# Performance work log

Hardware: AMD Instinct MI355X
Metric: run time of the kernel (lower is better)

The kernel has to match this reference:

```python
import jax, jax.numpy as jnp
import numpy as np

N_NODES = 50000
N_EDGES = 800000
F_IN = 128
F_OUT = 128
DROP_RATE = 0.6  # torch F.dropout(p=0.6, training=True default)


def setup_inputs() -> dict:
    key = jax.random.key(0)
    k1, k2, k3, k4, k5, k6 = jax.random.split(key, 6)
    x = jax.random.normal(k1, (N_NODES, F_IN), dtype=jnp.float32)
    # edge list: src = center node (sorted, mimics per-node neighbor-list grouping), dst = neighbor
    src = jnp.sort(jax.random.randint(k2, (N_EDGES,), 0, N_NODES, dtype=jnp.int64))
    dst = jax.random.randint(k3, (N_EDGES,), 0, N_NODES, dtype=jnp.int64)
    adj_vals = jax.random.uniform(k4, (N_EDGES,), dtype=jnp.float32)  # normalized adj weights
    stdv = 1.0 / np.sqrt(F_OUT)
    w_mask = jax.random.normal(k5, (2 * F_IN, F_IN), dtype=jnp.float32) * stdv
    w0 = jax.random.uniform(k6, (F_IN, F_OUT), minval=-stdv, maxval=stdv, dtype=jnp.float32)
    return {"x": x, "src": src, "dst": dst, "adj_vals": adj_vals, "w_mask": w_mask, "w0": w0}


def reference(x, src, dst, adj_vals, w_mask, w0):
    # Edge-wise gather of center and neighbor features: [E, F] each
    cen = x[src]
    nei = x[dst]
    # Per-edge mask: sigmoid(concat(center, neighbor) @ W_mask)  -> [E, F]
    m = jax.nn.sigmoid(jnp.concatenate([cen, nei], axis=1) @ w_mask)
    # Dropout p=0.6 (deterministic key for reproducibility), torch-style inverted scaling
    keep = jax.random.bernoulli(jax.random.key(42), 1.0 - DROP_RATE, m.shape)
    m = jnp.where(keep, m / (1.0 - DROP_RATE), jnp.zeros_like(m))
    # Masked weighted neighbor sum per center node, plus the center feature itself
    agg = jax.ops.segment_sum(m * nei, src, num_segments=N_NODES)
    x_new = x + agg
    # Dense projection, then spmm(adj, support) over the same edge structure
    support = x_new @ w0
    out = jax.ops.segment_sum(adj_vals[:, None] * support[dst], src, num_segments=N_NODES)
    return out
```

## Files before the change

kernel.cpp:

```cpp
#include <hip/hip_runtime.h>
#include <stdint.h>


#define NNODES 50000
#define FDIM 128

__device__ __forceinline__ uint32_t rotl32(uint32_t x, int r) {
  return (x << r) | (x >> (32 - r));
}

__device__ __forceinline__ void threefry2x32(uint32_t k0, uint32_t k1,
                                             uint32_t x0, uint32_t x1,
                                             uint32_t& o0, uint32_t& o1) {
  uint32_t k2 = k0 ^ k1 ^ 0x1BD11BDAu;
  x0 += k0; x1 += k1;
  x0 += x1; x1 = rotl32(x1, 13); x1 ^= x0;
  x0 += x1; x1 = rotl32(x1, 15); x1 ^= x0;
  x0 += x1; x1 = rotl32(x1, 26); x1 ^= x0;
  x0 += x1; x1 = rotl32(x1,  6); x1 ^= x0;
  x0 += k1; x1 += k2 + 1u;
  x0 += x1; x1 = rotl32(x1, 17); x1 ^= x0;
  x0 += x1; x1 = rotl32(x1, 29); x1 ^= x0;
  x0 += x1; x1 = rotl32(x1, 16); x1 ^= x0;
  x0 += x1; x1 = rotl32(x1, 24); x1 ^= x0;
  x0 += k2; x1 += k0 + 2u;
  x0 += x1; x1 = rotl32(x1, 13); x1 ^= x0;
  x0 += x1; x1 = rotl32(x1, 15); x1 ^= x0;
  x0 += x1; x1 = rotl32(x1, 26); x1 ^= x0;
  x0 += x1; x1 = rotl32(x1,  6); x1 ^= x0;
  x0 += k0; x1 += k1 + 3u;
  x0 += x1; x1 = rotl32(x1, 17); x1 ^= x0;
  x0 += x1; x1 = rotl32(x1, 29); x1 ^= x0;
  x0 += x1; x1 = rotl32(x1, 16); x1 ^= x0;
  x0 += x1; x1 = rotl32(x1, 24); x1 ^= x0;
  x0 += k1; x1 += k2 + 4u;
  x0 += x1; x1 = rotl32(x1, 13); x1 ^= x0;
  x0 += x1; x1 = rotl32(x1, 15); x1 ^= x0;
  x0 += x1; x1 = rotl32(x1, 26); x1 ^= x0;
  x0 += x1; x1 = rotl32(x1,  6); x1 ^= x0;
  x0 += k2; x1 += k0 + 5u;
  o0 = x0; o1 = x1;
}

__device__ __forceinline__ bool keep_drop(uint32_t idx) {
  uint32_t o0, o1;
  threefry2x32(0u, 42u, 0u, idx, o0, o1);
  return (o0 ^ o1) < 1717987328u;
}

__device__ __forceinline__ float sigmoid_f(float z) {
  float e = __builtin_amdgcn_exp2f(z * -1.44269504088896340736f);
  return __builtin_amdgcn_rcpf(1.0f + e);
}

__device__ __forceinline__ bool detect_i64(const int* p, int n) {
  int i = (n / 2) | 1;
  return p[i] == 0 && p[i + 2] == 0 && p[i + 4] == 0;
}

__device__ __forceinline__ int idx_at(const void* p, int i, bool is64) {
  return is64 ? (int)((const long long*)p)[i] : ((const int*)p)[i];
}

__device__ __forceinline__ int lower_bound_idx(const void* a, int n, bool is64, int v) {
  int lo = 0, hi = n;
  while (lo < hi) {
    int mid = (lo + hi) >> 1;
    if (idx_at(a, mid, is64) < v) lo = mid + 1; else hi = mid;
  }
  return lo;
}

__global__ __launch_bounds__(256) void rowptr_kernel(const void* __restrict__ src, int nE,
                                                     int* __restrict__ rowptr) {
  bool is64 = detect_i64((const int*)src, nE);
  int n = blockIdx.x * blockDim.x + threadIdx.x;
  if (n <= NNODES) rowptr[n] = lower_bound_idx(src, nE, is64, n);
}

__global__ __launch_bounds__(256) void cvt_dst(const void* __restrict__ dst, int nE,
                                               int* __restrict__ dst32) {
  bool is64 = detect_i64((const int*)dst, nE);
  int i = blockIdx.x * blockDim.x + threadIdx.x;
  if (i < nE) {
    int d = idx_at(dst, i, is64);
    dst32[i] = min(max(d, 0), NNODES - 1);
  }
}

#define MMR 16
__global__ __launch_bounds__(128) void matmulAB(const float* __restrict__ in,
                                                const float* __restrict__ W,
                                                float* __restrict__ A,
                                                float* __restrict__ B, int nrows) {
  __shared__ float xs[MMR][FDIM];
  int r0 = blockIdx.x * MMR;
  int t = threadIdx.x;
  #pragma unroll
  for (int r = 0; r < MMR; ++r) {
    int row = r0 + r;
    xs[r][t] = (row < nrows) ? in[row * FDIM + t] : 0.0f;
  }
  __syncthreads();
  float accA[MMR] = {}, accB[MMR] = {};
  for (int k = 0; k < FDIM; k += 4) {
    float wa0 = W[(k + 0) * FDIM + t], wa1 = W[(k + 1) * FDIM + t];
    float wa2 = W[(k + 2) * FDIM + t], wa3 = W[(k + 3) * FDIM + t];
    float wb0 = W[(FDIM + k + 0) * FDIM + t], wb1 = W[(FDIM + k + 1) * FDIM + t];
    float wb2 = W[(FDIM + k + 2) * FDIM + t], wb3 = W[(FDIM + k + 3) * FDIM + t];
    #pragma unroll
    for (int r = 0; r < MMR; ++r) {
      float4 xv = *(const float4*)&xs[r][k];
      accA[r] += xv.x * wa0; accA[r] += xv.y * wa1;
      accA[r] += xv.z * wa2; accA[r] += xv.w * wa3;
      accB[r] += xv.x * wb0; accB[r] += xv.y * wb1;
      accB[r] += xv.z * wb2; accB[r] += xv.w * wb3;
    }
  }
  #pragma unroll
  for (int r = 0; r < MMR; ++r) {
    int row = r0 + r;
    if (row < nrows) { A[row * FDIM + t] = accA[r]; B[row * FDIM + t] = accB[r]; }
  }
}

__global__ __launch_bounds__(128) void matmul16(const float* __restrict__ in,
                                                const float* __restrict__ W,
                                                float* __restrict__ out, int nrows) {
  __shared__ float xs[MMR][FDIM];
  int r0 = blockIdx.x * MMR;
  int t = threadIdx.x;
  #pragma unroll
  for (int r = 0; r < MMR; ++r) {
    int row = r0 + r;
    xs[r][t] = (row < nrows) ? in[row * FDIM + t] : 0.0f;
  }
  __syncthreads();
  float acc[MMR] = {};
  for (int k = 0; k < FDIM; k += 4) {
    float w0 = W[(k + 0) * FDIM + t], w1 = W[(k + 1) * FDIM + t];
    float w2 = W[(k + 2) * FDIM + t], w3 = W[(k + 3) * FDIM + t];
    #pragma unroll
    for (int r = 0; r < MMR; ++r) {
      float4 xv = *(const float4*)&xs[r][k];
      acc[r] += xv.x * w0; acc[r] += xv.y * w1;
      acc[r] += xv.z * w2; acc[r] += xv.w * w3;
    }
  }
  #pragma unroll
  for (int r = 0; r < MMR; ++r) {
    int row = r0 + r;
    if (row < nrows) out[row * FDIM + t] = acc[r];
  }
}

__global__ __launch_bounds__(128) void edge_agg(const float* __restrict__ x,
                                                const int* __restrict__ dst32,
                                                const int* __restrict__ rowptr,
                                                const float* __restrict__ A,
                                                const float* __restrict__ B,
                                                float* __restrict__ x_new) {
  int n = blockIdx.x;
  int f = threadIdx.x;
  int lo = rowptr[n], hi = rowptr[n + 1];
  const float* Bf = B + f;
  const float* xf = x + f;
  float a = A[(n << 7) + f];
  float acc0 = 0.f, acc1 = 0.f, acc2 = 0.f, acc3 = 0.f;
  uint32_t idx = ((uint32_t)lo << 7) + (uint32_t)f;
  int e = lo;
  for (; e + 4 <= hi; e += 4, idx += 512u) {
    int d0 = dst32[e + 0], d1 = dst32[e + 1], d2 = dst32[e + 2], d3 = dst32[e + 3];
    float b0 = Bf[d0 << 7], xv0 = xf[d0 << 7];
    float b1 = Bf[d1 << 7], xv1 = xf[d1 << 7];
    float b2 = Bf[d2 << 7], xv2 = xf[d2 << 7];
    float b3 = Bf[d3 << 7], xv3 = xf[d3 << 7];
    bool k0 = keep_drop(idx);
    bool k1 = keep_drop(idx + 128u);
    bool k2 = keep_drop(idx + 256u);
    bool k3 = keep_drop(idx + 384u);
    float m0 = sigmoid_f(a + b0), m1 = sigmoid_f(a + b1);
    float m2 = sigmoid_f(a + b2), m3 = sigmoid_f(a + b3);
    acc0 += k0 ? (m0 * 2.5f) * xv0 : 0.0f;
    acc1 += k1 ? (m1 * 2.5f) * xv1 : 0.0f;
    acc2 += k2 ? (m2 * 2.5f) * xv2 : 0.0f;
    acc3 += k3 ? (m3 * 2.5f) * xv3 : 0.0f;
  }
  for (; e < hi; ++e, idx += 128u) {
    int d = dst32[e];
    float m = sigmoid_f(a + Bf[d << 7]);
    if (keep_drop(idx)) acc0 += (m * 2.5f) * xf[d << 7];
  }
  float acc = (acc0 + acc1) + (acc2 + acc3);
  x_new[(n << 7) + f] = x[(n << 7) + f] + acc;
}

__global__ __launch_bounds__(128) void edge_out(const float* __restrict__ support,
                                                const int* __restrict__ dst32,
                                                const int* __restrict__ rowptr,
                                                const float* __restrict__ adj,
                                                float* __restrict__ out) {
  int n = blockIdx.x;
  int f = threadIdx.x;
  int lo = rowptr[n], hi = rowptr[n + 1];
  const float* Sf = support + f;
  float a0 = 0.f, a1 = 0.f, a2 = 0.f, a3 = 0.f;
  int e = lo;
  for (; e + 4 <= hi; e += 4) {
    int d0 = dst32[e + 0], d1 = dst32[e + 1], d2 = dst32[e + 2], d3 = dst32[e + 3];
    float w0 = adj[e + 0], w1 = adj[e + 1], w2 = adj[e + 2], w3 = adj[e + 3];
    a0 += w0 * Sf[d0 << 7];
    a1 += w1 * Sf[d1 << 7];
    a2 += w2 * Sf[d2 << 7];
    a3 += w3 * Sf[d3 << 7];
  }
  for (; e < hi; ++e) a0 += adj[e] * Sf[dst32[e] << 7];
  out[(n << 7) + f] = (a0 + a1) + (a2 + a3);
}

extern "C" void kernel_launch(void* const* d_in, const int* in_sizes, int n_in,
                              void* d_out, int out_size, void* d_ws, size_t ws_size,
                              hipStream_t stream) {
  const float* x      = (const float*)d_in[0];
  const void*  src    = d_in[1];
  const void*  dst    = d_in[2];
  const float* adj    = (const float*)d_in[3];
  const float* w_mask = (const float*)d_in[4];
  const float* w0     = (const float*)d_in[5];
  float* out = (float*)d_out;

  int nE = in_sizes[1];
  const size_t NF = (size_t)NNODES * FDIM;

  float* A       = (float*)d_ws;
  float* B       = A + NF;
  float* x_new   = B + NF;
  int*   rowptr  = (int*)(x_new + NF);
  int*   dst32   = rowptr + (NNODES + 1);
  float* support = A;

  rowptr_kernel<<<(NNODES + 256) / 256, 256, 0, stream>>>(src, nE, rowptr);
  cvt_dst<<<(nE + 255) / 256, 256, 0, stream>>>(dst, nE, dst32);
  matmulAB<<<(NNODES + MMR - 1) / MMR, 128, 0, stream>>>(x, w_mask, A, B, NNODES);
  edge_agg<<<NNODES, 128, 0, stream>>>(x, dst32, rowptr, A, B, x_new);
  matmul16<<<(NNODES + MMR - 1) / MMR, 128, 0, stream>>>(x_new, w0, support, NNODES);
  edge_out<<<NNODES, 128, 0, stream>>>(support, dst32, rowptr, adj, out);
}
```

Before: 505.0 us.

## Interleave mask logits with features and software-pipeline edge gathers

The mask matmul now writes B and x interleaved as float2, so the edge aggregation fetches both neighbor values with one 8-byte load instead of two scattered 4-byte loads. Both edge kernels use readfirstlane to keep row bounds and neighbor indices scalar, and prefetch the next batch of gathers (4 edges in aggregation, 8 in output) before computing the current one. Launch bounds now request higher occupancy. This needs extra workspace, with a fallback path when the workspace is too small, and the prefetch registers may limit occupancy.

```diff
diff --git a/kernel.cpp b/kernel.cpp
--- a/kernel.cpp
+++ b/kernel.cpp
@@ -53,6 +53,8 @@
   return __builtin_amdgcn_rcpf(1.0f + e);
 }
 
+__device__ __forceinline__ int rfl(int v) { return __builtin_amdgcn_readfirstlane(v); }
+
 __device__ __forceinline__ bool detect_i64(const int* p, int n) {
   int i = (n / 2) | 1;
   return p[i] == 0 && p[i + 2] == 0 && p[i + 4] == 0;
@@ -89,10 +91,11 @@
 }
 
 #define MMR 16
-__global__ __launch_bounds__(128) void matmulAB(const float* __restrict__ in,
-                                                const float* __restrict__ W,
-                                                float* __restrict__ A,
-                                                float* __restrict__ B, int nrows) {
+template <bool USE_BX>
+__global__ __launch_bounds__(128) void matmulAB_k(const float* __restrict__ in,
+                                                  const float* __restrict__ W,
+                                                  float* __restrict__ A,
+                                                  float* __restrict__ Bout, int nrows) {
   __shared__ float xs[MMR][FDIM];
   int r0 = blockIdx.x * MMR;
   int t = threadIdx.x;
@@ -120,7 +123,11 @@
   #pragma unroll
   for (int r = 0; r < MMR; ++r) {
     int row = r0 + r;
-    if (row < nrows) { A[row * FDIM + t] = accA[r]; B[row * FDIM + t] = accB[r]; }
+    if (row < nrows) {
+      A[row * FDIM + t] = accA[r];
+      if (USE_BX) ((float2*)Bout)[(row << 7) + t] = make_float2(accB[r], xs[r][t]);
+      else        Bout[row * FDIM + t] = accB[r];
+    }
   }
 }
 
@@ -154,67 +161,121 @@
   }
 }
 
-__global__ __launch_bounds__(128) void edge_agg(const float* __restrict__ x,
-                                                const int* __restrict__ dst32,
-                                                const int* __restrict__ rowptr,
-                                                const float* __restrict__ A,
-                                                const float* __restrict__ B,
-                                                float* __restrict__ x_new) {
+template <bool USE_BX>
+__global__ __launch_bounds__(128, 4) void edge_agg_k(const float* __restrict__ x,
+                                                     const float* __restrict__ BorBX,
+                                                     const int* __restrict__ dst32,
+                                                     const int* __restrict__ rowptr,
+                                                     const float* __restrict__ A,
+                                                     float* __restrict__ x_new) {
   int n = blockIdx.x;
   int f = threadIdx.x;
-  int lo = rowptr[n], hi = rowptr[n + 1];
-  const float* Bf = B + f;
-  const float* xf = x + f;
+  int lo = rfl(rowptr[n]);
+  int hi = rfl(rowptr[n + 1]);
+  const float2* BX2 = (const float2*)BorBX;
+  const float*  Bf  = BorBX + f;
+  const float*  xf  = x + f;
   float a = A[(n << 7) + f];
   float acc0 = 0.f, acc1 = 0.f, acc2 = 0.f, acc3 = 0.f;
-  uint32_t idx = ((uint32_t)lo << 7) + (uint32_t)f;
   int e = lo;
-  for (; e + 4 <= hi; e += 4, idx += 512u) {
-    int d0 = dst32[e + 0], d1 = dst32[e + 1], d2 = dst32[e + 2], d3 = dst32[e + 3];
-    float b0 = Bf[d0 << 7], xv0 = xf[d0 << 7];
-    float b1 = Bf[d1 << 7], xv1 = xf[d1 << 7];
-    float b2 = Bf[d2 << 7], xv2 = xf[d2 << 7];
-    float b3 = Bf[d3 << 7], xv3 = xf[d3 << 7];
-    bool k0 = keep_drop(idx);
-    bool k1 = keep_drop(idx + 128u);
-    bool k2 = keep_drop(idx + 256u);
-    bool k3 = keep_drop(idx + 384u);
-    float m0 = sigmoid_f(a + b0), m1 = sigmoid_f(a + b1);
-    float m2 = sigmoid_f(a + b2), m3 = sigmoid_f(a + b3);
-    acc0 += k0 ? (m0 * 2.5f) * xv0 : 0.0f;
-    acc1 += k1 ? (m1 * 2.5f) * xv1 : 0.0f;
-    acc2 += k2 ? (m2 * 2.5f) * xv2 : 0.0f;
-    acc3 += k3 ? (m3 * 2.5f) * xv3 : 0.0f;
-  }
-  for (; e < hi; ++e, idx += 128u) {
-    int d = dst32[e];
-    float m = sigmoid_f(a + Bf[d << 7]);
-    if (keep_drop(idx)) acc0 += (m * 2.5f) * xf[d << 7];
-  }
-  float acc = (acc0 + acc1) + (acc2 + acc3);
-  x_new[(n << 7) + f] = x[(n << 7) + f] + acc;
-}
-
-__global__ __launch_bounds__(128) void edge_out(const float* __restrict__ support,
-                                                const int* __restrict__ dst32,
-                                                const int* __restrict__ rowptr,
-                                                const float* __restrict__ adj,
-                                                float* __restrict__ out) {
+  if (hi - lo >= 4) {
+    float2 v0, v1, v2, v3;
+    {
+      int d0 = rfl(dst32[e]), d1 = rfl(dst32[e + 1]);
+      int d2 = rfl(dst32[e + 2]), d3 = rfl(dst32[e + 3]);
+      if (USE_BX) {
+        v0 = BX2[(d0 << 7) + f]; v1 = BX2[(d1 << 7) + f];
+        v2 = BX2[(d2 << 7) + f]; v3 = BX2[(d3 << 7) + f];
+      } else {
+        v0 = make_float2(Bf[d0 << 7], xf[d0 << 7]);
+        v1 = make_float2(Bf[d1 << 7], xf[d1 << 7]);
+        v2 = make_float2(Bf[d2 << 7], xf[d2 << 7]);
+        v3 = make_float2(Bf[d3 << 7], xf[d3 << 7]);
+      }
+    }
+    for (; e + 4 <= hi;) {
+      int ne = (e + 8 <= hi) ? e + 4 : e;
+      int nd0 = rfl(dst32[ne]), nd1 = rfl(dst32[ne + 1]);
+      int nd2 = rfl(dst32[ne + 2]), nd3 = rfl(dst32[ne + 3]);
+      float2 w0, w1, w2, w3;
+      if (USE_BX) {
+        w0 = BX2[(nd0 << 7) + f]; w1 = BX2[(nd1 << 7) + f];
+        w2 = BX2[(nd2 << 7) + f]; w3 = BX2[(nd3 << 7) + f];
+      } else {
+        w0 = make_float2(Bf[nd0 << 7], xf[nd0 << 7]);
+        w1 = make_float2(Bf[nd1 << 7], xf[nd1 << 7]);
+        w2 = make_float2(Bf[nd2 << 7], xf[nd2 << 7]);
+        w3 = make_float2(Bf[nd3 << 7], xf[nd3 << 7]);
+      }
+      uint32_t idx = ((uint32_t)e << 7) + (uint32_t)f;
+      bool k0 = keep_drop(idx);
+      bool k1 = keep_drop(idx + 128u);
+      bool k2 = keep_drop(idx + 256u);
+      bool k3 = keep_drop(idx + 384u);
+      float m0 = sigmoid_f(a + v0.x), m1 = sigmoid_f(a + v1.x);
+      float m2 = sigmoid_f(a + v2.x), m3 = sigmoid_f(a + v3.x);
+      acc0 += k0 ? (m0 * 2.5f) * v0.y : 0.0f;
+      acc1 += k1 ? (m1 * 2.5f) * v1.y : 0.0f;
+      acc2 += k2 ? (m2 * 2.5f) * v2.y : 0.0f;
+      acc3 += k3 ? (m3 * 2.5f) * v3.y : 0.0f;
+      v0 = w0; v1 = w1; v2 = w2; v3 = w3;
+      e += 4;
+    }
+  }
+  for (; e < hi; ++e) {
+    int d = rfl(dst32[e]);
+    uint32_t idx = ((uint32_t)e << 7) + (uint32_t)f;
+    float bb, xx;
+    if (USE_BX) { float2 v = BX2[(d << 7) + f]; bb = v.x; xx = v.y; }
+    else        { bb = Bf[d << 7]; xx = xf[d << 7]; }
+    float m = sigmoid_f(a + bb);
+    if (keep_drop(idx)) acc0 += (m * 2.5f) * xx;
+  }
+  x_new[(n << 7) + f] = x[(n << 7) + f] + ((acc0 + acc1) + (acc2 + acc3));
+}
+
+__global__ __launch_bounds__(128, 4) void edge_out(const float* __restrict__ support,
+                                                   const int* __restrict__ dst32,
+                                                   const int* __restrict__ rowptr,
+                                                   const float* __restrict__ adj,
+                                                   float* __restrict__ out) {
   int n = blockIdx.x;
   int f = threadIdx.x;
-  int lo = rowptr[n], hi = rowptr[n + 1];
+  int lo = rfl(rowptr[n]), hi = rfl(rowptr[n + 1]);
   const float* Sf = support + f;
   float a0 = 0.f, a1 = 0.f, a2 = 0.f, a3 = 0.f;
   int e = lo;
-  for (; e + 4 <= hi; e += 4) {
-    int d0 = dst32[e + 0], d1 = dst32[e + 1], d2 = dst32[e + 2], d3 = dst32[e + 3];
-    float w0 = adj[e + 0], w1 = adj[e + 1], w2 = adj[e + 2], w3 = adj[e + 3];
-    a0 += w0 * Sf[d0 << 7];
-    a1 += w1 * Sf[d1 << 7];
-    a2 += w2 * Sf[d2 << 7];
-    a3 += w3 * Sf[d3 << 7];
-  }
-  for (; e < hi; ++e) a0 += adj[e] * Sf[dst32[e] << 7];
+  if (hi - lo >= 8) {
+    float s0, s1, s2, s3, s4, s5, s6, s7;
+    float w0, w1, w2, w3, w4, w5, w6, w7;
+    {
+      int d0 = rfl(dst32[e]),     d1 = rfl(dst32[e + 1]);
+      int d2 = rfl(dst32[e + 2]), d3 = rfl(dst32[e + 3]);
+      int d4 = rfl(dst32[e + 4]), d5 = rfl(dst32[e + 5]);
+      int d6 = rfl(dst32[e + 6]), d7 = rfl(dst32[e + 7]);
+      s0 = Sf[d0 << 7]; s1 = Sf[d1 << 7]; s2 = Sf[d2 << 7]; s3 = Sf[d3 << 7];
+      s4 = Sf[d4 << 7]; s5 = Sf[d5 << 7]; s6 = Sf[d6 << 7]; s7 = Sf[d7 << 7];
+      w0 = adj[e]; w1 = adj[e + 1]; w2 = adj[e + 2]; w3 = adj[e + 3];
+      w4 = adj[e + 4]; w5 = adj[e + 5]; w6 = adj[e + 6]; w7 = adj[e + 7];
+    }
+    for (; e + 8 <= hi;) {
+      int ne = (e + 16 <= hi) ? e + 8 : e;
+      int nd0 = rfl(dst32[ne]),     nd1 = rfl(dst32[ne + 1]);
+      int nd2 = rfl(dst32[ne + 2]), nd3 = rfl(dst32[ne + 3]);
+      int nd4 = rfl(dst32[ne + 4]), nd5 = rfl(dst32[ne + 5]);
+      int nd6 = rfl(dst32[ne + 6]), nd7 = rfl(dst32[ne + 7]);
+      float t0 = Sf[nd0 << 7], t1 = Sf[nd1 << 7], t2 = Sf[nd2 << 7], t3 = Sf[nd3 << 7];
+      float t4 = Sf[nd4 << 7], t5 = Sf[nd5 << 7], t6 = Sf[nd6 << 7], t7 = Sf[nd7 << 7];
+      float u0 = adj[ne], u1 = adj[ne + 1], u2 = adj[ne + 2], u3 = adj[ne + 3];
+      float u4 = adj[ne + 4], u5 = adj[ne + 5], u6 = adj[ne + 6], u7 = adj[ne + 7];
+      a0 += w0 * s0; a1 += w1 * s1; a2 += w2 * s2; a3 += w3 * s3;
+      a0 += w4 * s4; a1 += w5 * s5; a2 += w6 * s6; a3 += w7 * s7;
+      s0 = t0; s1 = t1; s2 = t2; s3 = t3; s4 = t4; s5 = t5; s6 = t6; s7 = t7;
+      w0 = u0; w1 = u1; w2 = u2; w3 = u3; w4 = u4; w5 = u5; w6 = u6; w7 = u7;
+      e += 8;
+    }
+  }
+  for (; e < hi; ++e) a0 += adj[e] * Sf[rfl(dst32[e]) << 7];
   out[(n << 7) + f] = (a0 + a1) + (a2 + a3);
 }
 
@@ -232,17 +293,25 @@
   int nE = in_sizes[1];
   const size_t NF = (size_t)NNODES * FDIM;
 
-  float* A       = (float*)d_ws;
-  float* B       = A + NF;
-  float* x_new   = B + NF;
-  int*   rowptr  = (int*)(x_new + NF);
-  int*   dst32   = rowptr + (NNODES + 1);
+  size_t need_bx = (4 * NF + (size_t)(NNODES + 1) + (size_t)nE) * 4;
+  bool use_bx = ws_size >= need_bx;
+
+  float* A      = (float*)d_ws;
+  float* Bbuf   = A + NF;
+  float* x_new  = Bbuf + (use_bx ? 2 * NF : NF);
+  int*   rowptr = (int*)(x_new + NF);
+  int*   dst32  = rowptr + (NNODES + 1);
   float* support = A;
 
   rowptr_kernel<<<(NNODES + 256) / 256, 256, 0, stream>>>(src, nE, rowptr);
   cvt_dst<<<(nE + 255) / 256, 256, 0, stream>>>(dst, nE, dst32);
-  matmulAB<<<(NNODES + MMR - 1) / MMR, 128, 0, stream>>>(x, w_mask, A, B, NNODES);
-  edge_agg<<<NNODES, 128, 0, stream>>>(x, dst32, rowptr, A, B, x_new);
+  if (use_bx) {
+    matmulAB_k<true><<<(NNODES + MMR - 1) / MMR, 128, 0, stream>>>(x, w_mask, A, Bbuf, NNODES);
+    edge_agg_k<true><<<NNODES, 128, 0, stream>>>(x, Bbuf, dst32, rowptr, A, x_new);
+  } else {
+    matmulAB_k<false><<<(NNODES + MMR - 1) / MMR, 128, 0, stream>>>(x, w_mask, A, Bbuf, NNODES);
+    edge_agg_k<false><<<NNODES, 128, 0, stream>>>(x, Bbuf, dst32, rowptr, A, x_new);
+  }
   matmul16<<<(NNODES + MMR - 1) / MMR, 128, 0, stream>>>(x_new, w0, support, NNODES);
   edge_out<<<NNODES, 128, 0, stream>>>(support, dst32, rowptr, adj, out);
 }
```

After: 510.1 us. About the same (+1.0%).
